# Performance work log

Measured on AMD Instinct MI355X. Metric: run time of the kernel, lower is better.

The kernel has to match this reference:

```python
import jax, jax.numpy as jnp
import numpy as np

N_ATOMS = 200_000
N_EDGES = 4_000_000

# physical / numerical constants closed over by BambooBase
ELE_FACTOR = 332.0637  # Coulomb constant, kcal*A/mol/e^2
EWALD_F = 1.12837917   # 2/sqrt(pi)
EWALD_P = 0.3275911
EWALD_A = (0.254829592, -0.284496736, 1.421413741, -1.453152027, 1.061405429)
COUL_BETA = 18.7
COUL_R0 = 2.2
DISP_CUTOFF = 10.0
G_EWALD = 0.3          # typical Ewald splitting parameter (1/A)


def setup_inputs() -> dict:
    key = jax.random.key(0)
    k1, k2, k3, k4, k5, k6, k7 = jax.random.split(key, 7)
    row = jax.random.randint(k1, (N_EDGES,), 0, N_ATOMS, dtype=jnp.int32)
    col = jax.random.randint(k2, (N_EDGES,), 0, N_ATOMS, dtype=jnp.int32)
    # edge displacement vectors: random direction, radius in [1, 10) Angstrom
    direction = jax.random.normal(k3, (N_EDGES, 3), dtype=jnp.float32)
    direction = direction / jnp.linalg.norm(direction, axis=-1, keepdims=True)
    radius = jax.random.uniform(k4, (N_EDGES, 1), minval=1.0, maxval=10.0, dtype=jnp.float32)
    dij = direction * radius
    charge = 0.3 * jax.random.normal(k5, (N_ATOMS,), dtype=jnp.float32)
    c6 = jax.random.uniform(k6, (N_ATOMS,), minval=1.0, maxval=100.0, dtype=jnp.float32)
    r0 = jax.random.uniform(k7, (N_ATOMS,), minval=2.0, maxval=4.0, dtype=jnp.float32)
    return {"row": row, "col": col, "dij": dij, "charge": charge, "c6": c6, "r0": r0}


def reference(row, col, dij, charge, c6, r0):
    # ---- shared per-edge distance ----
    rij = jnp.sqrt(jnp.sum(dij * dij, axis=-1))  # [E]

    # ---- get_coulomb ----
    prefactor = ELE_FACTOR * charge[row] * charge[col] / rij
    damp = jax.nn.sigmoid(COUL_BETA / COUL_R0 * (rij - COUL_R0))
    # torch.nn.Softplus(beta=b)(x) == softplus(b*x)/b
    sp = jax.nn.softplus(COUL_BETA * (rij - COUL_R0) / COUL_R0) / COUL_BETA
    s = rij / COUL_R0 / (1.0 + sp)
    ecoul = prefactor * s
    fcoul = prefactor * damp * s * s
    # Ewald short-range correction (erfc via Horner polynomial)
    grij = G_EWALD * rij
    expm2 = jnp.exp(-grij * grij)
    t = 1.0 / (1.0 + EWALD_P * grij)
    a0, a1, a2, a3, a4 = EWALD_A
    erfc = t * (a0 + t * (a1 + t * (a2 + t * (a3 + t * a4)))) * expm2
    ecoul = ecoul + prefactor * (erfc - 1.0)
    fcoul = fcoul + prefactor * (erfc + EWALD_F * grij * expm2 - 1.0)
    coul_fij = dij * (fcoul / (rij * rij))[:, None]

    # ---- get_dispersion (D3-CSO) ----
    c6ij = jnp.sqrt(c6[row] * c6[col])
    r0ij = 0.5 * (r0[row] + r0[col])
    r6 = rij ** 6 + 4.5 ** 6
    e = jnp.exp(rij - 2.5 * r0ij)
    cso = 0.85 + 0.82 / (1.0 + e)
    edisp = -c6ij / r6 * cso
    fdisp = -6.0 * c6ij * rij ** 5 / (r6 * r6) * cso - c6ij / r6 * (0.82 * e / (1.0 + e) ** 2)
    disp_fij = dij * (fdisp / rij)[:, None]
    edisp = edisp + c6ij / DISP_CUTOFF ** 6

    return ecoul, coul_fij, edisp, disp_fij
```

## Files before the change

kernel.cpp:

```cpp
#include <hip/hip_runtime.h>
#include <math.h>

#define C_ELE   332.0637f
#define C_EWF   1.12837917f
#define C_EWP   0.3275911f
#define C_A0    0.254829592f
#define C_A1   -0.284496736f
#define C_A2    1.421413741f
#define C_A3   -1.453152027f
#define C_A4    1.061405429f
#define C_BETA  18.7f
#define C_R0    2.2f
#define C_GEW   0.3f
#define C_45P6  8303.765625f
#define C_DC6I  1e-6f

typedef float vf4 __attribute__((ext_vector_type(4)));
typedef int   vi4 __attribute__((ext_vector_type(4)));

__device__ __forceinline__ float frcp(float x) { return __builtin_amdgcn_rcpf(x); }

struct EdgeOut { float ec, fx, fy, fz, ed, gx, gy, gz; };

__device__ __forceinline__ EdgeOut edge_compute(
    vf4 ar, vf4 ac, float dx, float dy, float dz)
{
    float r2   = dx * dx + dy * dy + dz * dz;
    float rij  = sqrtf(r2);
    float rinv = frcp(rij);

    float pref = C_ELE * ar.x * ac.x * rinv;
    float x    = (C_BETA / C_R0) * (rij - C_R0);
    float ax   = fabsf(x);
    float ex   = __expf(-ax);
    float den  = frcp(1.0f + ex);
    float damp = (x >= 0.0f) ? den : ex * den;
    float sp   = (fmaxf(x, 0.0f) + __logf(1.0f + ex)) * (1.0f / C_BETA);
    float s    = rij * (1.0f / C_R0) * frcp(1.0f + sp);

    float grij  = C_GEW * rij;
    float expm2 = __expf(-grij * grij);
    float t     = frcp(1.0f + C_EWP * grij);
    float erfc  = t * (C_A0 + t * (C_A1 + t * (C_A2 + t * (C_A3 + t * C_A4)))) * expm2;

    EdgeOut o;
    o.ec = pref * (s + erfc - 1.0f);
    float fcl = pref * (damp * s * s + erfc + C_EWF * grij * expm2 - 1.0f);
    float fsc = fcl * frcp(r2);
    o.fx = dx * fsc; o.fy = dy * fsc; o.fz = dz * fsc;

    float c6ij  = sqrtf(ar.y * ac.y);
    float r0ij  = 0.5f * (ar.z + ac.z);
    float r6    = r2 * r2 * r2 + C_45P6;
    float r6i   = frcp(r6);
    float e     = __expf(rij - 2.5f * r0ij);
    float onep  = frcp(1.0f + e);
    float cso   = 0.85f + 0.82f * onep;
    o.ed = -c6ij * r6i * cso + c6ij * C_DC6I;
    float r5  = r2 * r2 * rij;
    float fd  = -6.0f * c6ij * r5 * r6i * r6i * cso - c6ij * r6i * (0.82f * e * onep * onep);
    float gsc = fd * rinv;
    o.gx = dx * gsc; o.gy = dy * gsc; o.gz = dz * gsc;
    return o;
}

__global__ __launch_bounds__(256) void pack_atoms(
    const float* __restrict__ charge, const float* __restrict__ c6a,
    const float* __restrict__ r0a, vf4* __restrict__ tbl, int N)
{
    int i = blockIdx.x * blockDim.x + threadIdx.x;
    if (i < N) {
        vf4 v = { charge[i], c6a[i], r0a[i], 0.0f };
        tbl[i] = v;
    }
}

__global__ __launch_bounds__(256) void bamboo_lds(
    const int* __restrict__ row, const int* __restrict__ col,
    const float* __restrict__ dij,
    const vf4* __restrict__ tbl,
    float* __restrict__ out, int E)
{
    __shared__ float s_dij[256 * 13];
    __shared__ float s_cf [256 * 13];
    __shared__ float s_df [256 * 13];

    const int t     = threadIdx.x;
    const int ebase = blockIdx.x << 10;
    const int gbase = ebase + t * 4;

    float* __restrict__ ec_o = out;
    float* __restrict__ cf_o = out + (size_t)E;
    float* __restrict__ ed_o = out + (size_t)4 * E;
    float* __restrict__ df_o = out + (size_t)5 * E;

    vi4 rr = __builtin_nontemporal_load((const vi4*)(row + gbase));
    vi4 cc = __builtin_nontemporal_load((const vi4*)(col + gbase));

    const vf4* dstream = (const vf4*)(dij + (size_t)ebase * 3);
    vf4 d0 = __builtin_nontemporal_load(dstream + (0 * 256 + t));
    vf4 d1 = __builtin_nontemporal_load(dstream + (1 * 256 + t));
    vf4 d2 = __builtin_nontemporal_load(dstream + (2 * 256 + t));
    __builtin_amdgcn_sched_barrier(0);

    vf4 a0r = tbl[rr.x]; vf4 a0c = tbl[cc.x];
    vf4 a1r = tbl[rr.y]; vf4 a1c = tbl[cc.y];
    vf4 a2r = tbl[rr.z]; vf4 a2c = tbl[cc.z];
    vf4 a3r = tbl[rr.w]; vf4 a3c = tbl[cc.w];
    __builtin_amdgcn_sched_barrier(0);

    {
        int v, q, r, b;
        v = 0 * 256 + t; q = v / 3; r = v - 3 * q; b = q * 13 + 4 * r;
        s_dij[b + 0] = d0.x; s_dij[b + 1] = d0.y; s_dij[b + 2] = d0.z; s_dij[b + 3] = d0.w;
        v = 1 * 256 + t; q = v / 3; r = v - 3 * q; b = q * 13 + 4 * r;
        s_dij[b + 0] = d1.x; s_dij[b + 1] = d1.y; s_dij[b + 2] = d1.z; s_dij[b + 3] = d1.w;
        v = 2 * 256 + t; q = v / 3; r = v - 3 * q; b = q * 13 + 4 * r;
        s_dij[b + 0] = d2.x; s_dij[b + 1] = d2.y; s_dij[b + 2] = d2.z; s_dij[b + 3] = d2.w;
    }
    __syncthreads();

    float d[12];
    #pragma unroll
    for (int m = 0; m < 12; ++m) d[m] = s_dij[t * 13 + m];

    EdgeOut o0 = edge_compute(a0r, a0c, d[0],  d[1],  d[2]);
    EdgeOut o1 = edge_compute(a1r, a1c, d[3],  d[4],  d[5]);
    EdgeOut o2 = edge_compute(a2r, a2c, d[6],  d[7],  d[8]);
    EdgeOut o3 = edge_compute(a3r, a3c, d[9],  d[10], d[11]);

    vf4 ec4 = { o0.ec, o1.ec, o2.ec, o3.ec };
    vf4 ed4 = { o0.ed, o1.ed, o2.ed, o3.ed };
    __builtin_nontemporal_store(ec4, (vf4*)(ec_o + gbase));
    __builtin_nontemporal_store(ed4, (vf4*)(ed_o + gbase));

    {
        float* cf = s_cf + t * 13;
        float* df = s_df + t * 13;
        cf[0]  = o0.fx; cf[1]  = o0.fy; cf[2]  = o0.fz;
        cf[3]  = o1.fx; cf[4]  = o1.fy; cf[5]  = o1.fz;
        cf[6]  = o2.fx; cf[7]  = o2.fy; cf[8]  = o2.fz;
        cf[9]  = o3.fx; cf[10] = o3.fy; cf[11] = o3.fz;
        df[0]  = o0.gx; df[1]  = o0.gy; df[2]  = o0.gz;
        df[3]  = o1.gx; df[4]  = o1.gy; df[5]  = o1.gz;
        df[6]  = o2.gx; df[7]  = o2.gy; df[8]  = o2.gz;
        df[9]  = o3.gx; df[10] = o3.gy; df[11] = o3.gz;
    }
    __syncthreads();

    vf4* cf_out = (vf4*)(cf_o + (size_t)ebase * 3);
    vf4* df_out = (vf4*)(df_o + (size_t)ebase * 3);
    #pragma unroll
    for (int j = 0; j < 3; ++j) {
        int v = j * 256 + t;
        int q = v / 3, r = v - 3 * q, b = q * 13 + 4 * r;
        vf4 wc = { s_cf[b], s_cf[b + 1], s_cf[b + 2], s_cf[b + 3] };
        __builtin_nontemporal_store(wc, cf_out + v);
        vf4 wd = { s_df[b], s_df[b + 1], s_df[b + 2], s_df[b + 3] };
        __builtin_nontemporal_store(wd, df_out + v);
    }
}

__global__ __launch_bounds__(256) void bamboo_scalar(
    const int* __restrict__ row, const int* __restrict__ col,
    const float* __restrict__ dij,
    const float* __restrict__ charge, const float* __restrict__ c6a,
    const float* __restrict__ r0a,
    float* __restrict__ out, int E, int start)
{
    int j = start + blockIdx.x * blockDim.x + threadIdx.x;
    if (j >= E) return;
    float* ec_o = out;
    float* cf_o = out + (size_t)E;
    float* ed_o = out + (size_t)4 * E;
    float* df_o = out + (size_t)5 * E;
    int r = row[j], c = col[j];
    vf4 ar = { charge[r], c6a[r], r0a[r], 0.0f };
    vf4 ac = { charge[c], c6a[c], r0a[c], 0.0f };
    EdgeOut o = edge_compute(ar, ac,
                             dij[3 * (size_t)j], dij[3 * (size_t)j + 1], dij[3 * (size_t)j + 2]);
    ec_o[j] = o.ec; ed_o[j] = o.ed;
    cf_o[3 * (size_t)j] = o.fx; cf_o[3 * (size_t)j + 1] = o.fy; cf_o[3 * (size_t)j + 2] = o.fz;
    df_o[3 * (size_t)j] = o.gx; df_o[3 * (size_t)j + 1] = o.gy; df_o[3 * (size_t)j + 2] = o.gz;
}

extern "C" void kernel_launch(void* const* d_in, const int* in_sizes, int n_in,
                              void* d_out, int out_size, void* d_ws, size_t ws_size,
                              hipStream_t stream) {
    const int*   row    = (const int*)d_in[0];
    const int*   col    = (const int*)d_in[1];
    const float* dij    = (const float*)d_in[2];
    const float* charge = (const float*)d_in[3];
    const float* c6a    = (const float*)d_in[4];
    const float* r0a    = (const float*)d_in[5];
    float* out = (float*)d_out;
    int E = in_sizes[0];
    int N = in_sizes[3];

    size_t need = (size_t)N * sizeof(vf4);
    if (ws_size >= need && ((uintptr_t)d_ws % 16) == 0) {
        vf4* tbl = (vf4*)d_ws;
        pack_atoms<<<(N + 255) / 256, 256, 0, stream>>>(charge, c6a, r0a, tbl, N);
        int ntiles = E >> 10;
        int tail   = ntiles << 10;
        if (ntiles > 0)
            bamboo_lds<<<ntiles, 256, 0, stream>>>(row, col, dij, tbl, out, E);
        if (tail < E)
            bamboo_scalar<<<(E - tail + 255) / 256, 256, 0, stream>>>(
                row, col, dij, charge, c6a, r0a, out, E, tail);
    } else {
        bamboo_scalar<<<(E + 255) / 256, 256, 0, stream>>>(row, col, dij, charge, c6a, r0a, out, E, 0);
    }
}
```

Before: 231.2 us.

## Pack atom table to 8 bytes with fp16 c6/r0, reuse LDS, fold tail

The per-atom gather table shrinks from 16 to 8 bytes by storing c6 and r0 as packed fp16 next to the fp32 charge. This halves the random-gather footprint so more of the 200k-atom table fits in cache. The two output staging buffers in shared memory are merged into the input buffer to cut LDS use, and launch bounds now request 4 blocks per CU. The tail edges are handled inside block 0 instead of a separate launch. The fp16 rounding of c6 and r0 reduces accuracy of the dispersion terms.

```diff
diff --git a/kernel.cpp b/kernel.cpp
--- a/kernel.cpp
+++ b/kernel.cpp
@@ -15,12 +15,21 @@
 #define C_45P6  8303.765625f
 #define C_DC6I  1e-6f
 
-typedef float vf4 __attribute__((ext_vector_type(4)));
-typedef int   vi4 __attribute__((ext_vector_type(4)));
+typedef float  vf4 __attribute__((ext_vector_type(4)));
+typedef int    vi4 __attribute__((ext_vector_type(4)));
+typedef int    vi2 __attribute__((ext_vector_type(2)));
+typedef __fp16 vh2 __attribute__((ext_vector_type(2)));
 
 __device__ __forceinline__ float frcp(float x) { return __builtin_amdgcn_rcpf(x); }
 
 struct EdgeOut { float ec, fx, fy, fz, ed, gx, gy, gz; };
+
+__device__ __forceinline__ vf4 unpack8(vi2 v)
+{
+    union { int i; vh2 h; } u; u.i = v.y;
+    vf4 r = { __int_as_float(v.x), (float)u.h.x, (float)u.h.y, 0.0f };
+    return r;
+}
 
 __device__ __forceinline__ EdgeOut edge_compute(
     vf4 ar, vf4 ac, float dx, float dy, float dz)
@@ -64,26 +73,27 @@
     return o;
 }
 
-__global__ __launch_bounds__(256) void pack_atoms(
+__global__ __launch_bounds__(256) void pack_atoms8(
     const float* __restrict__ charge, const float* __restrict__ c6a,
-    const float* __restrict__ r0a, vf4* __restrict__ tbl, int N)
+    const float* __restrict__ r0a, vi2* __restrict__ tbl, int N)
 {
     int i = blockIdx.x * blockDim.x + threadIdx.x;
     if (i < N) {
-        vf4 v = { charge[i], c6a[i], r0a[i], 0.0f };
+        vh2 h = __builtin_amdgcn_cvt_pkrtz(c6a[i], r0a[i]);
+        union { vh2 h; int i; } u; u.h = h;
+        vi2 v = { __float_as_int(charge[i]), u.i };
         tbl[i] = v;
     }
 }
 
-__global__ __launch_bounds__(256) void bamboo_lds(
+__global__ __launch_bounds__(256, 4) void bamboo_lds8(
     const int* __restrict__ row, const int* __restrict__ col,
     const float* __restrict__ dij,
-    const vf4* __restrict__ tbl,
+    const vi2* __restrict__ tbl,
     float* __restrict__ out, int E)
 {
-    __shared__ float s_dij[256 * 13];
-    __shared__ float s_cf [256 * 13];
-    __shared__ float s_df [256 * 13];
+    __shared__ float s_a[256 * 13];
+    __shared__ float s_b[256 * 13];
 
     const int t     = threadIdx.x;
     const int ebase = blockIdx.x << 10;
@@ -103,31 +113,32 @@
     vf4 d2 = __builtin_nontemporal_load(dstream + (2 * 256 + t));
     __builtin_amdgcn_sched_barrier(0);
 
-    vf4 a0r = tbl[rr.x]; vf4 a0c = tbl[cc.x];
-    vf4 a1r = tbl[rr.y]; vf4 a1c = tbl[cc.y];
-    vf4 a2r = tbl[rr.z]; vf4 a2c = tbl[cc.z];
-    vf4 a3r = tbl[rr.w]; vf4 a3c = tbl[cc.w];
+    vi2 g0r = tbl[rr.x]; vi2 g0c = tbl[cc.x];
+    vi2 g1r = tbl[rr.y]; vi2 g1c = tbl[cc.y];
+    vi2 g2r = tbl[rr.z]; vi2 g2c = tbl[cc.z];
+    vi2 g3r = tbl[rr.w]; vi2 g3c = tbl[cc.w];
     __builtin_amdgcn_sched_barrier(0);
 
     {
         int v, q, r, b;
         v = 0 * 256 + t; q = v / 3; r = v - 3 * q; b = q * 13 + 4 * r;
-        s_dij[b + 0] = d0.x; s_dij[b + 1] = d0.y; s_dij[b + 2] = d0.z; s_dij[b + 3] = d0.w;
+        s_a[b + 0] = d0.x; s_a[b + 1] = d0.y; s_a[b + 2] = d0.z; s_a[b + 3] = d0.w;
         v = 1 * 256 + t; q = v / 3; r = v - 3 * q; b = q * 13 + 4 * r;
-        s_dij[b + 0] = d1.x; s_dij[b + 1] = d1.y; s_dij[b + 2] = d1.z; s_dij[b + 3] = d1.w;
+        s_a[b + 0] = d1.x; s_a[b + 1] = d1.y; s_a[b + 2] = d1.z; s_a[b + 3] = d1.w;
         v = 2 * 256 + t; q = v / 3; r = v - 3 * q; b = q * 13 + 4 * r;
-        s_dij[b + 0] = d2.x; s_dij[b + 1] = d2.y; s_dij[b + 2] = d2.z; s_dij[b + 3] = d2.w;
+        s_a[b + 0] = d2.x; s_a[b + 1] = d2.y; s_a[b + 2] = d2.z; s_a[b + 3] = d2.w;
     }
     __syncthreads();
 
     float d[12];
     #pragma unroll
-    for (int m = 0; m < 12; ++m) d[m] = s_dij[t * 13 + m];
-
-    EdgeOut o0 = edge_compute(a0r, a0c, d[0],  d[1],  d[2]);
-    EdgeOut o1 = edge_compute(a1r, a1c, d[3],  d[4],  d[5]);
-    EdgeOut o2 = edge_compute(a2r, a2c, d[6],  d[7],  d[8]);
-    EdgeOut o3 = edge_compute(a3r, a3c, d[9],  d[10], d[11]);
+    for (int m = 0; m < 12; ++m) d[m] = s_a[t * 13 + m];
+    __syncthreads();
+
+    EdgeOut o0 = edge_compute(unpack8(g0r), unpack8(g0c), d[0], d[1],  d[2]);
+    EdgeOut o1 = edge_compute(unpack8(g1r), unpack8(g1c), d[3], d[4],  d[5]);
+    EdgeOut o2 = edge_compute(unpack8(g2r), unpack8(g2c), d[6], d[7],  d[8]);
+    EdgeOut o3 = edge_compute(unpack8(g3r), unpack8(g3c), d[9], d[10], d[11]);
 
     vf4 ec4 = { o0.ec, o1.ec, o2.ec, o3.ec };
     vf4 ed4 = { o0.ed, o1.ed, o2.ed, o3.ed };
@@ -135,8 +146,8 @@
     __builtin_nontemporal_store(ed4, (vf4*)(ed_o + gbase));
 
     {
-        float* cf = s_cf + t * 13;
-        float* df = s_df + t * 13;
+        float* cf = s_b + t * 13;
+        float* df = s_a + t * 13;
         cf[0]  = o0.fx; cf[1]  = o0.fy; cf[2]  = o0.fz;
         cf[3]  = o1.fx; cf[4]  = o1.fy; cf[5]  = o1.fz;
         cf[6]  = o2.fx; cf[7]  = o2.fy; cf[8]  = o2.fz;
@@ -154,10 +165,23 @@
     for (int j = 0; j < 3; ++j) {
         int v = j * 256 + t;
         int q = v / 3, r = v - 3 * q, b = q * 13 + 4 * r;
-        vf4 wc = { s_cf[b], s_cf[b + 1], s_cf[b + 2], s_cf[b + 3] };
+        vf4 wc = { s_b[b], s_b[b + 1], s_b[b + 2], s_b[b + 3] };
         __builtin_nontemporal_store(wc, cf_out + v);
-        vf4 wd = { s_df[b], s_df[b + 1], s_df[b + 2], s_df[b + 3] };
+        vf4 wd = { s_a[b], s_a[b + 1], s_a[b + 2], s_a[b + 3] };
         __builtin_nontemporal_store(wd, df_out + v);
+    }
+
+    if (blockIdx.x == 0) {
+        for (int j = ((int)gridDim.x << 10) + t; j < E; j += 256) {
+            vi2 vr = tbl[row[j]];
+            vi2 vc = tbl[col[j]];
+            EdgeOut o = edge_compute(unpack8(vr), unpack8(vc),
+                                     dij[3 * (size_t)j], dij[3 * (size_t)j + 1],
+                                     dij[3 * (size_t)j + 2]);
+            ec_o[j] = o.ec; ed_o[j] = o.ed;
+            cf_o[3 * (size_t)j] = o.fx; cf_o[3 * (size_t)j + 1] = o.fy; cf_o[3 * (size_t)j + 2] = o.fz;
+            df_o[3 * (size_t)j] = o.gx; df_o[3 * (size_t)j + 1] = o.gy; df_o[3 * (size_t)j + 2] = o.gz;
+        }
     }
 }
 
@@ -197,17 +221,12 @@
     int E = in_sizes[0];
     int N = in_sizes[3];
 
-    size_t need = (size_t)N * sizeof(vf4);
-    if (ws_size >= need && ((uintptr_t)d_ws % 16) == 0) {
-        vf4* tbl = (vf4*)d_ws;
-        pack_atoms<<<(N + 255) / 256, 256, 0, stream>>>(charge, c6a, r0a, tbl, N);
-        int ntiles = E >> 10;
-        int tail   = ntiles << 10;
-        if (ntiles > 0)
-            bamboo_lds<<<ntiles, 256, 0, stream>>>(row, col, dij, tbl, out, E);
-        if (tail < E)
-            bamboo_scalar<<<(E - tail + 255) / 256, 256, 0, stream>>>(
-                row, col, dij, charge, c6a, r0a, out, E, tail);
+    size_t need = (size_t)N * sizeof(vi2);
+    int ntiles = E >> 10;
+    if (ws_size >= need && ((uintptr_t)d_ws % 8) == 0 && ntiles > 0) {
+        vi2* tbl = (vi2*)d_ws;
+        pack_atoms8<<<(N + 255) / 256, 256, 0, stream>>>(charge, c6a, r0a, tbl, N);
+        bamboo_lds8<<<ntiles, 256, 0, stream>>>(row, col, dij, tbl, out, E);
     } else {
         bamboo_scalar<<<(E + 255) / 256, 256, 0, stream>>>(row, col, dij, charge, c6a, r0a, out, E, 0);
     }
```

After: 229.6 us. No clear change (-0.7%).
